# Kernel optimization log

Hardware: AMD Instinct MI355X
Metric: run time of the kernel (lower is better)

Reference implementation:

```python
import jax, jax.numpy as jnp
import numpy as np

DIM = 1024; DEPTH = 4; HEADS = 16; DIM_HEAD = 64
INNER = HEADS * DIM_HEAD            # 1024
N_LAT = 64; N_MP = 4; MAX_SEQ = 512
FF_MULT = 4; HID = DIM * FF_MULT    # 4096
B = 32; SEQ = 512
EPS = 1e-5


def _custom_ln(x, g):
    # LayerNorm with gain only (module's custom LayerNorm), biased variance
    mean = x.mean(-1, keepdims=True)
    var = x.var(-1, keepdims=True)
    return (x - mean) * jax.lax.rsqrt(var + EPS) * g


def _std_ln(x, w, b):
    # torch nn.LayerNorm with weight and bias
    mean = x.mean(-1, keepdims=True)
    var = x.var(-1, keepdims=True)
    return (x - mean) * jax.lax.rsqrt(var + EPS) * w + b


def setup_inputs() -> dict:
    key = jax.random.key(0)
    ks = jax.random.split(key, 12)
    w = lambda k, shape: jax.random.normal(k, shape, jnp.float32) * 0.02
    return {
        "x": jax.random.normal(ks[0], (B, SEQ, DIM), jnp.float32),
        "mask": jnp.ones((B, SEQ), dtype=bool),
        "pos_emb": w(ks[1], (MAX_SEQ, DIM)),
        "latents": jax.random.normal(ks[2], (N_LAT, DIM), jnp.float32),
        "mp_ln_g": jnp.ones((DIM,), jnp.float32),
        "mp_w": w(ks[3], (DIM, DIM * N_MP)),
        "mp_b": jnp.zeros((DIM * N_MP,), jnp.float32),
        "attn_norm_w": jnp.ones((DEPTH, DIM), jnp.float32),
        "attn_norm_b": jnp.zeros((DEPTH, DIM), jnp.float32),
        "attn_lat_w": jnp.ones((DEPTH, DIM), jnp.float32),
        "attn_lat_b": jnp.zeros((DEPTH, DIM), jnp.float32),
        "Wq": w(ks[4], (DEPTH, DIM, INNER)),
        "Wkv": w(ks[5], (DEPTH, DIM, 2 * INNER)),
        "Wout": w(ks[6], (DEPTH, INNER, DIM)),
        "out_ln_w": jnp.ones((DEPTH, DIM), jnp.float32),
        "out_ln_b": jnp.zeros((DEPTH, DIM), jnp.float32),
        "ff_ln1_g": jnp.ones((DEPTH, DIM), jnp.float32),
        "ff_w1": w(ks[7], (DEPTH, DIM, HID)),
        "ff_ln2_g": jnp.ones((DEPTH, HID), jnp.float32),
        "ff_w2": w(ks[8], (DEPTH, HID, DIM)),
    }


def _forward(x, mask, pos_emb, latents, mp_ln_g, mp_w, mp_b,
             attn_norm_w, attn_norm_b, attn_lat_w, attn_lat_b,
             Wq, Wkv, Wout, out_ln_w, out_ln_b,
             ff_ln1_g, ff_w1, ff_ln2_g, ff_w2):
    b, n, d = x.shape
    x_pos = x + pos_emb[:n]                              # [b, n, d]
    lat = jnp.broadcast_to(latents, (b,) + latents.shape)  # [b, 64, d]

    # latents from mean-pooled sequence (mask in torch code is all-ones)
    pooled = x.mean(axis=1)                              # [b, d]
    mp_lat = (_custom_ln(pooled, mp_ln_g) @ mp_w + mp_b).reshape(b, N_MP, d)
    lat = jnp.concatenate([mp_lat, lat], axis=1)         # [b, 68, d]
    n_lat = lat.shape[1]

    scale = DIM_HEAD ** -0.5
    pad_mask = jnp.pad(mask, ((0, 0), (0, n_lat)), constant_values=True)  # [b, n+68]
    neg = -jnp.finfo(jnp.float32).max

    def split_heads(t):
        return t.reshape(b, -1, HEADS, DIM_HEAD).transpose(0, 2, 1, 3)  # b h n d

    for i in range(DEPTH):
        # --- PerceiverAttention ---
        xn = _std_ln(x_pos, attn_norm_w[i], attn_norm_b[i])
        ln_ = _std_ln(lat, attn_lat_w[i], attn_lat_b[i])
        q = split_heads(ln_ @ Wq[i]) * scale
        kv = jnp.concatenate([xn, ln_], axis=1) @ Wkv[i]   # [b, n+68, 2*inner]
        k, v = jnp.split(kv, 2, axis=-1)
        k = split_heads(k); v = split_heads(v)
        sim = jnp.einsum('bhid,bhjd->bhij', q, k)          # [b, h, 68, n+68]
        sim = jnp.where(pad_mask[:, None, None, :], sim, neg)
        attn = jax.nn.softmax(sim.astype(jnp.float32), axis=-1).astype(sim.dtype)
        out = jnp.einsum('bhij,bhjd->bhid', attn, v)
        out = out.transpose(0, 2, 1, 3).reshape(b, n_lat, INNER)
        lat = _std_ln(out @ Wout[i], out_ln_w[i], out_ln_b[i]) + lat
        # --- FeedForward ---
        h = _custom_ln(lat, ff_ln1_g[i]) @ ff_w1[i]
        h = jax.nn.gelu(h, approximate=False)              # torch nn.GELU default
        h = _custom_ln(h, ff_ln2_g[i]) @ ff_w2[i]
        lat = h + lat
    return lat


def reference(x, mask, pos_emb, latents, mp_ln_g, mp_w, mp_b,
              attn_norm_w, attn_norm_b, attn_lat_w, attn_lat_b,
              Wq, Wkv, Wout, out_ln_w, out_ln_b,
              ff_ln1_g, ff_w1, ff_ln2_g, ff_w2):
    return _forward(x, mask, pos_emb, latents, mp_ln_g, mp_w, mp_b,
                    attn_norm_w, attn_norm_b, attn_lat_w, attn_lat_b,
                    Wq, Wkv, Wout, out_ln_w, out_ln_b,
                    ff_ln1_g, ff_w1, ff_ln2_g, ff_w2)
```

## Files before the change

### kernel.cpp

```cpp
#include <hip/hip_runtime.h>


typedef __attribute__((ext_vector_type(4))) float f32x4;
typedef __attribute__((ext_vector_type(8))) __bf16 bf16x8;
typedef __attribute__((ext_vector_type(4))) __bf16 bf16x4;

#define BATCH 32
#define SEQL  512
#define DIM   1024
#define HEADS 16
#define DH    64
#define LTOT  68
#define KEYS  580
#define KPAD  640
#define HID   4096
#define LN_EPS 1e-5f
#define MLAT  2176

__device__ __forceinline__ float bf2f(__bf16 v) { return (float)v; }
__device__ __forceinline__ __bf16 f2bf(float v) { return (__bf16)v; }
__device__ __forceinline__ float gelu_f(float v) {
    return 0.5f * v * (1.0f + erff(v * 0.70710678118654752f));
}

__device__ __forceinline__ void gld_lds16(const __bf16* g, __bf16* l) {
    __builtin_amdgcn_global_load_lds(
        (const __attribute__((address_space(1))) void*)g,
        (__attribute__((address_space(3))) void*)l, 16, 0, 0);
}

#define SBAR()   asm volatile("s_barrier" ::: "memory")
#define VMCNT4() asm volatile("s_waitcnt vmcnt(4)" ::: "memory")

__device__ __forceinline__ void block_reduce2(float& a, float& b, float* red) {
#pragma unroll
    for (int m = 32; m > 0; m >>= 1) {
        a += __shfl_xor(a, m, 64);
        b += __shfl_xor(b, m, 64);
    }
    int wid = threadIdx.x >> 6, lane = threadIdx.x & 63;
    __syncthreads();
    if (lane == 0) { red[wid] = a; red[4 + wid] = b; }
    __syncthreads();
    a = red[0] + red[1] + red[2] + red[3];
    b = red[4] + red[5] + red[6] + red[7];
}

__global__ __launch_bounds__(256) void add_pos(const float* __restrict__ x,
                                               const float* __restrict__ pos,
                                               __bf16* __restrict__ xp) {
    const int total4 = (BATCH * SEQL * DIM) / 4;
    const int pos4m = (SEQL * DIM) / 4 - 1;
    for (int i = blockIdx.x * 256 + threadIdx.x; i < total4; i += gridDim.x * 256) {
        f32x4 xv = ((const f32x4*)x)[i];
        f32x4 pv = ((const f32x4*)pos)[i & pos4m];
        bf16x4 o;
#pragma unroll
        for (int j = 0; j < 4; ++j) o[j] = f2bf(xv[j] + pv[j]);
        ((bf16x4*)xp)[i] = o;
    }
}

__global__ __launch_bounds__(256) void pool_mean(const float* __restrict__ x,
                                                 float* __restrict__ pooled) {
    int b = blockIdx.x >> 2;
    int d = ((blockIdx.x & 3) << 8) + threadIdx.x;
    const float* p = x + (size_t)b * SEQL * DIM + d;
    float s = 0.f;
    for (int ss = 0; ss < SEQL; ++ss) s += p[(size_t)ss * DIM];
    pooled[b * DIM + d] = s * (1.f / SEQL);
}

__global__ __launch_bounds__(256) void lat_fill(const float* __restrict__ latents,
                                                float* __restrict__ lat) {
    int i = blockIdx.x * 256 + threadIdx.x;
    int b = i >> 14;
    int rem = i & 16383;
    int r = rem >> 8, d4 = rem & 255;
    ((f32x4*)lat)[(size_t)(b * LTOT + 4 + r) * 256 + d4] = ((const f32x4*)latents)[rem];
}

template <typename Tin, bool STD, int COLS>
__global__ __launch_bounds__(256) void ln_rows(const Tin* __restrict__ in,
                                               __bf16* __restrict__ out,
                                               const float* __restrict__ w,
                                               const float* __restrict__ bb) {
    __shared__ float red[8];
    constexpr int NPT = COLS / 256;
    size_t base = (size_t)blockIdx.x * COLS;
    int t = threadIdx.x;
    int c0 = t * NPT;
    float xv[NPT];
    float s = 0.f, s2 = 0.f;
#pragma unroll
    for (int k4 = 0; k4 < NPT / 4; ++k4) {
        if constexpr (sizeof(Tin) == 2) {
            bf16x4 v = *(const bf16x4*)(in + base + c0 + k4 * 4);
#pragma unroll
            for (int e = 0; e < 4; ++e) {
                float f = bf2f(v[e]);
                xv[k4 * 4 + e] = f; s += f; s2 += f * f;
            }
        } else {
            f32x4 v = *(const f32x4*)((const float*)in + base + c0 + k4 * 4);
#pragma unroll
            for (int e = 0; e < 4; ++e) {
                float f = v[e];
                xv[k4 * 4 + e] = f; s += f; s2 += f * f;
            }
        }
    }
    block_reduce2(s, s2, red);
    float mean = s * (1.f / COLS);
    float var = s2 * (1.f / COLS) - mean * mean;
    float rstd = rsqrtf(var + LN_EPS);
#pragma unroll
    for (int k4 = 0; k4 < NPT / 4; ++k4) {
        f32x4 wv = *(const f32x4*)(w + c0 + k4 * 4);
        f32x4 bv;
        if (STD) bv = *(const f32x4*)(bb + c0 + k4 * 4);
        bf16x4 o;
#pragma unroll
        for (int e = 0; e < 4; ++e) {
            float y = (xv[k4 * 4 + e] - mean) * rstd * wv[e];
            if (STD) y += bv[e];
            o[e] = f2bf(y);
        }
        *(bf16x4*)(out + base + c0 + k4 * 4) = o;
    }
}

__global__ __launch_bounds__(256) void ln_gelu2(const __bf16* __restrict__ pk,
                                                __bf16* __restrict__ out,
                                                const float* __restrict__ g) {
    __shared__ float red[8];
    constexpr int NPT = HID / 256;
    const size_t S = (size_t)MLAT * HID;
    size_t base = (size_t)blockIdx.x * HID;
    int t = threadIdx.x;
    int c0 = t * NPT;
    float xv[NPT];
    float s = 0.f, s2 = 0.f;
#pragma unroll
    for (int k4 = 0; k4 < NPT / 4; ++k4) {
        bf16x4 va = *(const bf16x4*)(pk + base + c0 + k4 * 4);
        bf16x4 vb = *(const bf16x4*)(pk + S + base + c0 + k4 * 4);
#pragma unroll
        for (int e = 0; e < 4; ++e) {
            float f = gelu_f(bf2f(va[e]) + bf2f(vb[e]));
            xv[k4 * 4 + e] = f; s += f; s2 += f * f;
        }
    }
    block_reduce2(s, s2, red);
    float mean = s * (1.f / HID);
    float var = s2 * (1.f / HID) - mean * mean;
    float rstd = rsqrtf(var + LN_EPS);
#pragma unroll
    for (int k4 = 0; k4 < NPT / 4; ++k4) {
        f32x4 gv = *(const f32x4*)(g + c0 + k4 * 4);
        bf16x4 o;
#pragma unroll
        for (int e = 0; e < 4; ++e)
            o[e] = f2bf((xv[k4 * 4 + e] - mean) * rstd * gv[e]);
        *(bf16x4*)(out + base + c0 + k4 * 4) = o;
    }
}

__global__ __launch_bounds__(256) void wout_ln_res(const __bf16* __restrict__ gin,
                                                   float* __restrict__ lat,
                                                   __bf16* __restrict__ ffin,
                                                   const float* __restrict__ w,
                                                   const float* __restrict__ b,
                                                   const float* __restrict__ g1) {
    __shared__ float red[8];
    const size_t SL = (size_t)MLAT * DIM;
    size_t base = (size_t)blockIdx.x * DIM;
    int t = threadIdx.x;
    float xv[4];
    float s = 0.f, s2 = 0.f;
#pragma unroll
    for (int k = 0; k < 4; ++k) {
        size_t idx = base + t + (k << 8);
        float v = bf2f(gin[idx]) + bf2f(gin[idx + SL]) +
                  bf2f(gin[idx + 2 * SL]) + bf2f(gin[idx + 3 * SL]);
        xv[k] = v; s += v; s2 += v * v;
    }
    block_reduce2(s, s2, red);
    float mean = s * (1.f / DIM);
    float var = s2 * (1.f / DIM) - mean * mean;
    float rstd = rsqrtf(var + LN_EPS);
    float yv[4];
    s = 0.f; s2 = 0.f;
#pragma unroll
    for (int k = 0; k < 4; ++k) {
        int c = t + (k << 8);
        float y = (xv[k] - mean) * rstd * w[c] + b[c] + lat[base + c];
        yv[k] = y; s += y; s2 += y * y;
        lat[base + c] = y;
    }
    block_reduce2(s, s2, red);
    float mean2 = s * (1.f / DIM);
    float var2 = s2 * (1.f / DIM) - mean2 * mean2;
    float rstd2 = rsqrtf(var2 + LN_EPS);
#pragma unroll
    for (int k = 0; k < 4; ++k) {
        int c = t + (k << 8);
        ffin[base + c] = f2bf((yv[k] - mean2) * rstd2 * g1[c]);
    }
}

__global__ __launch_bounds__(256) void qkv_red(const __bf16* __restrict__ pk,
                                               __bf16* __restrict__ qb,
                                               __bf16* __restrict__ kvb) {
    const size_t S = (size_t)MLAT * 3072;
    int row = blockIdx.y;
    int n = (blockIdx.x * 256 + threadIdx.x) * 4;
    size_t idx = (size_t)row * 3072 + n;
    bf16x4 a = *(const bf16x4*)(pk + idx);
    bf16x4 b = *(const bf16x4*)(pk + S + idx);
    bf16x4 o;
    if (n < 1024) {
#pragma unroll
        for (int e = 0; e < 4; ++e) o[e] = f2bf((bf2f(a[e]) + bf2f(b[e])) * 0.125f);
        *(bf16x4*)(qb + (size_t)row * 1024 + n) = o;
    } else {
#pragma unroll
        for (int e = 0; e < 4; ++e) o[e] = f2bf(bf2f(a[e]) + bf2f(b[e]));
        int bb = ((row >> 2) * 61681) >> 20;
        int r = row - bb * 68;
        *(bf16x4*)(kvb + (size_t)bb * KEYS * 2048 + (size_t)(512 + r) * 2048 +
                   (n - 1024)) = o;
    }
}

__global__ __launch_bounds__(256) void splitk_add8(const __bf16* __restrict__ p,
                                                   float* __restrict__ lat) {
    const size_t S = (size_t)MLAT * 1024;
    int i = blockIdx.x * 256 + threadIdx.x;
    size_t e0 = (size_t)i * 4;
    f32x4 acc = ((f32x4*)lat)[i];
#pragma unroll
    for (int s = 0; s < 8; ++s) {
        bf16x4 v = *(const bf16x4*)(p + s * S + e0);
#pragma unroll
        for (int e = 0; e < 4; ++e) acc[e] += bf2f(v[e]);
    }
    ((f32x4*)lat)[i] = acc;
}

__global__ __launch_bounds__(256) void transpose_all(
    const float* __restrict__ Wq, const float* __restrict__ Wkv,
    const float* __restrict__ Wout, const float* __restrict__ f1,
    const float* __restrict__ f2,
    __bf16* __restrict__ wqT, __bf16* __restrict__ wkvT,
    __bf16* __restrict__ woutT, __bf16* __restrict__ f1T,
    __bf16* __restrict__ f2T) {
    __shared__ float tile[32][33];
    int bid = blockIdx.x;
    const float* in; __bf16* out; int N, nxs, ti;
    if (bid < 1024)      { in = Wq;  out = wqT;  N = 1024; nxs = 5; ti = bid; }
    else if (bid < 3072) { in = Wkv; out = wkvT; N = 2048; nxs = 6; ti = bid - 1024; }
    else if (bid < 4096) { in = Wout;out = woutT;N = 1024; nxs = 5; ti = bid - 3072; }
    else if (bid < 8192) { in = f1;  out = f1T;  N = 4096; nxs = 7; ti = bid - 4096; }
    else                 { in = f2;  out = f2T;  N = 1024; nxs = 5; ti = bid - 8192; }
    int K = (bid >= 8192) ? 4096 : 1024;
    int n0 = (ti & ((1 << nxs) - 1)) << 5;
    int k0 = (ti >> nxs) << 5;
    int tx = threadIdx.x & 31, ty = threadIdx.x >> 5;
#pragma unroll
    for (int p = 0; p < 4; ++p) {
        int kk = ty + p * 8;
        tile[kk][tx] = in[(size_t)(k0 + kk) * N + n0 + tx];
    }
    __syncthreads();
#pragma unroll
    for (int p = 0; p < 4; ++p) {
        int nn = ty + p * 8;
        out[(size_t)(n0 + nn) * K + k0 + tx] = f2bf(tile[tx][nn]);
    }
}

__global__ __launch_bounds__(256) void transpose_cast(const float* __restrict__ in,
                                                      __bf16* __restrict__ out,
                                                      int K, int N) {
    __shared__ float tile[32][33];
    int n0 = blockIdx.x * 32, k0 = blockIdx.y * 32;
    int tx = threadIdx.x & 31, ty = threadIdx.x >> 5;
#pragma unroll
    for (int p = 0; p < 4; ++p) {
        int kk = ty + p * 8;
        tile[kk][tx] = in[(size_t)(k0 + kk) * N + n0 + tx];
    }
    __syncthreads();
#pragma unroll
    for (int p = 0; p < 4; ++p) {
        int nn = ty + p * 8;
        out[(size_t)(n0 + nn) * K + k0 + tx] = f2bf(tile[tx][nn]);
    }
}

template <int EPI, bool POW2>
__global__ __launch_bounds__(256) void gemm_bf16(
    const __bf16* __restrict__ A, const __bf16* __restrict__ Bt,
    void* __restrict__ C0, void* __restrict__ C1, const float* __restrict__ bias,
    int M, int N, int K, int lda, int ldb, int brs, long long bstride, int ldc,
    float scale, int az, long long cz, int zhalf) {
    __shared__ __bf16 As[128][64];
    __shared__ __bf16 Bs[128][64];
    const int t = threadIdx.x;
    const int m0 = blockIdx.y * 128, n0 = blockIdx.x * 128;
    const int z = blockIdx.z;
    A += (size_t)z * az;
    Bt += (size_t)z * az;
    void* Cout = (z < zhalf) ? C0 : C1;
    const long long zoff = (long long)(z < zhalf ? z : z - zhalf) * cz;
    const int wid = t >> 6, lane = t & 63;
    const int wr = wid >> 1, wc = wid & 1;
    const int lrow = lane & 15;
    const int lr = lane >> 3, lc = lane & 7;
    const int src_col = (lc ^ lr) << 3;
    f32x4 acc[4][4] = {};

    int garow[4], gbrow[4];
#pragma unroll
    for (int it = 0; it < 4; ++it) {
        int r = wid * 8 + it * 32 + lr;
        int gm = m0 + r; garow[it] = gm < M ? gm : M - 1;
        int gn = n0 + r; gbrow[it] = gn < N ? gn : N - 1;
    }

    for (int kt = 0; kt < K; kt += 64) {
#pragma unroll
        for (int it = 0; it < 4; ++it) {
            int rb = wid * 8 + it * 32;
            gld_lds16(A + (size_t)garow[it] * lda + kt + src_col, &As[rb][0]);
            gld_lds16(Bt + (size_t)gbrow[it] * ldb + kt + src_col, &Bs[rb][0]);
        }
        __syncthreads();
#pragma unroll
        for (int kc = 0; kc < 2; ++kc) {
            const int ck = (kc << 2) + (lane >> 4);
            bf16x8 af[4], bfr[4];
#pragma unroll
            for (int f = 0; f < 4; ++f) {
                int ra = wr * 64 + f * 16 + lrow;
                af[f] = *(const bf16x8*)(&As[ra][(ck ^ (ra & 7)) << 3]);
                int rb = wc * 64 + f * 16 + lrow;
                bfr[f] = *(const bf16x8*)(&Bs[rb][(ck ^ (rb & 7)) << 3]);
            }
#pragma unroll
            for (int fm = 0; fm < 4; ++fm)
#pragma unroll
                for (int fn = 0; fn < 4; ++fn)
                    acc[fm][fn] = __builtin_amdgcn_mfma_f32_16x16x32_bf16(
                        af[fm], bfr[fn], acc[fm][fn], 0, 0, 0);
        }
        __syncthreads();
    }
    const int rbase = (lane >> 4) << 2;
    const int cofs = lane & 15;
    const int msk = POW2 ? (int)((1u << brs) - 1u) : 0;
#pragma unroll
    for (int fm = 0; fm < 4; ++fm) {
#pragma unroll
        for (int j = 0; j < 4; ++j) {
            int m = m0 + wr * 64 + fm * 16 + rbase + j;
            if (m >= M) continue;
            long long roff;
            if (POW2) roff = (long long)(m >> brs) * bstride + (long long)(m & msk) * ldc;
            else      roff = (long long)(m / brs) * bstride + (long long)(m % brs) * ldc;
            roff += zoff;
#pragma unroll
            for (int fn = 0; fn < 4; ++fn) {
                int n = n0 + wc * 64 + fn * 16 + cofs;
                if (n >= N) continue;
                float v = acc[fm][fn][j];
                if (bias) v += bias[n];
                if (EPI == 0) ((float*)Cout)[roff + n] = v;
                else if (EPI == 1) ((__bf16*)Cout)[roff + n] = f2bf(v);
                else if (EPI == 2) ((__bf16*)Cout)[roff + n] = f2bf(v * scale);
                else ((float*)Cout)[roff + n] = gelu_f(v);
            }
        }
    }
}

template <int EPI>
__global__ __launch_bounds__(512, 2) void gemm256(
    const __bf16* __restrict__ A, const __bf16* __restrict__ Bt,
    void* __restrict__ Cout, const float* __restrict__ bias,
    int M, int N, int K, int brs, long long bstride, int ldc, float scale,
    int gxs) {
    __shared__ __bf16 As[2][256][64];
    __shared__ __bf16 Bs[2][256][64];
    const int t = threadIdx.x;
    const int wid = t >> 6, lane = t & 63;
    const int wr = wid >> 2, wc = wid & 3;
    const int lrow = lane & 15, lk = lane >> 4;
    const int lr8 = lane >> 3;
    const int scol = ((lane & 7) ^ lr8) << 3;

    int nwg = gridDim.x;
    int L = blockIdx.x;
    if ((nwg & 7) == 0) L = (L & 7) * (nwg >> 3) + (L >> 3);
    const int bx = L & ((1 << gxs) - 1), by = L >> gxs;
    const int m0 = by * 256, n0 = bx * 256;

    unsigned aoff[4], boff[4];
#pragma unroll
    for (int h = 0; h < 2; ++h)
#pragma unroll
        for (int rnd = 0; rnd < 2; ++rnd) {
            int r = h * 128 + rnd * 64 + wid * 8 + lr8;
            int gm = m0 + r; if (gm > M - 1) gm = M - 1;
            aoff[h * 2 + rnd] = (unsigned)(gm * K + scol);
            int gn = n0 + r; if (gn > N - 1) gn = N - 1;
            boff[h * 2 + rnd] = (unsigned)(gn * K + scol);
        }

    auto stgA = [&](int buf, int tile, int h) {
        int kt = tile << 6;
        gld_lds16(A + aoff[h * 2 + 0] + kt, &As[buf][h * 128 + wid * 8][0]);
        gld_lds16(A + aoff[h * 2 + 1] + kt, &As[buf][h * 128 + 64 + wid * 8][0]);
    };
    auto stgB = [&](int buf, int tile, int h) {
        int kt = tile << 6;
        gld_lds16(Bt + boff[h * 2 + 0] + kt, &Bs[buf][h * 128 + wid * 8][0]);
        gld_lds16(Bt + boff[h * 2 + 1] + kt, &Bs[buf][h * 128 + 64 + wid * 8][0]);
    };

    f32x4 acc[8][4] = {};
    bf16x8 AF0[4][2], AF1[4][2], BF[2][2], BF2[2][2];

    auto rdAF = [&](bf16x8 (&AF)[4][2], int buf, int qm) {
#pragma unroll
        for (int i = 0; i < 4; ++i) {
            int ra = wr * 128 + (qm * 4 + i) * 16 + lrow;
            AF[i][0] = *(const bf16x8*)(&As[buf][ra][((lk) ^ (ra & 7)) << 3]);
            AF[i][1] = *(const bf16x8*)(&As[buf][ra][((4 + lk) ^ (ra & 7)) << 3]);
        }
    };
    auto rdBF = [&](bf16x8 (&BV)[2][2], int buf, int qn) {
#pragma unroll
        for (int i = 0; i < 2; ++i) {
            int rb = wc * 64 + (qn * 2 + i) * 16 + lrow;
            BV[i][0] = *(const bf16x8*)(&Bs[buf][rb][((lk) ^ (rb & 7)) << 3]);
            BV[i][1] = *(const bf16x8*)(&Bs[buf][rb][((4 + lk) ^ (rb & 7)) << 3]);
        }
    };
    auto mfq = [&](bf16x8 (&AF)[4][2], bf16x8 (&BV)[2][2], int mo, int no) {
        __builtin_amdgcn_s_setprio(1);
#pragma unroll
        for (int i = 0; i < 4; ++i)
#pragma unroll
            for (int nf = 0; nf < 2; ++nf)
#pragma unroll
                for (int ks = 0; ks < 2; ++ks)
                    acc[mo + i][no + nf] = __builtin_amdgcn_mfma_f32_16x16x32_bf16(
                        AF[i][ks], BV[nf][ks], acc[mo + i][no + nf], 0, 0, 0);
        __builtin_amdgcn_s_setprio(0);
    };

    const int nt = K >> 6;
    stgA(0, 0, 0); stgA(0, 0, 1);
    stgB(0, 0, 0); stgB(0, 0, 1);
    stgA(1, 1, 0); stgA(1, 1, 1);
    VMCNT4();
    SBAR();

    for (int tt = 0; tt < nt; tt += 2) {
        const int t1 = tt + 1;
        const int t2 = (tt + 2 < nt) ? tt + 2 : nt - 1;
        const int t3 = (tt + 3 < nt) ? tt + 3 : nt - 1;
        rdAF(AF0, 0, 0); rdBF(BF, 0, 0);
        stgB(1, t1, 0);
        SBAR();
        mfq(AF0, BF, 0, 0);
        SBAR();
        rdAF(AF1, 0, 1);
        stgB(1, t1, 1);
        SBAR();
        mfq(AF1, BF, 4, 0);
        SBAR();
        rdBF(BF2, 0, 1);
        stgA(0, t2, 0);
        SBAR();
        mfq(AF1, BF2, 4, 2);
        SBAR();
        stgA(0, t2, 1);
        SBAR();
        mfq(AF0, BF2, 0, 2);
        VMCNT4();
        SBAR();
        rdAF(AF0, 1, 0); rdBF(BF, 1, 0);
        stgB(0, t2, 0);
        SBAR();
        mfq(AF0, BF, 0, 0);
        SBAR();
        rdAF(AF1, 1, 1);
        stgB(0, t2, 1);
        SBAR();
        mfq(AF1, BF, 4, 0);
        SBAR();
        rdBF(BF2, 1, 1);
        stgA(1, t3, 0);
        SBAR();
        mfq(AF1, BF2, 4, 2);
        SBAR();
        stgA(1, t3, 1);
        SBAR();
        mfq(AF0, BF2, 0, 2);
        VMCNT4();
        SBAR();
    }

    const int rbase = (lane >> 4) << 2;
    const int cofs = lane & 15;
    const int msk = (int)((1u << brs) - 1u);
#pragma unroll
    for (int mf = 0; mf < 8; ++mf) {
#pragma unroll
        for (int j = 0; j < 4; ++j) {
            int m = m0 + wr * 128 + mf * 16 + rbase + j;
            if (m >= M) continue;
            long long roff = (long long)(m >> brs) * bstride +
                             (long long)(m & msk) * ldc;
#pragma unroll
            for (int nf = 0; nf < 4; ++nf) {
                int n = n0 + wc * 64 + nf * 16 + cofs;
                if (n >= N) continue;
                float v = acc[mf][nf][j];
                if (bias) v += bias[n];
                if (EPI == 1) ((__bf16*)Cout)[roff + n] = f2bf(v);
                else if (EPI == 3) ((float*)Cout)[roff + n] = gelu_f(v);
                else ((float*)Cout)[roff + n] = v;
            }
        }
    }
}

__global__ __launch_bounds__(256) void qk_gemm(const __bf16* __restrict__ q,
                                               const __bf16* __restrict__ kv,
                                               __bf16* __restrict__ sp) {
    __shared__ __bf16 Qs[80][64];
    __shared__ __bf16 Ks[128][64];
    const int bh = blockIdx.x, b = bh >> 4, h = bh & 15;
    const int n0 = blockIdx.y * 128;
    const int t = threadIdx.x, wid = t >> 6, lane = t & 63;
    const __bf16* qbase = q + (size_t)b * LTOT * DIM + h * DH;
    const __bf16* kbase = kv + (size_t)b * KEYS * 2048 + h * DH;
    const bf16x8 zero8 = {};

    for (int s = t; s < 80 * 8; s += 256) {
        int r = s >> 3, c8 = s & 7;
        bf16x8 v = zero8;
        if (r < LTOT) v = *(const bf16x8*)(qbase + (size_t)r * DIM + (c8 << 3));
        *(bf16x8*)(&Qs[r][(c8 ^ (r & 7)) << 3]) = v;
    }
    for (int s = t; s < 128 * 8; s += 256) {
        int r = s >> 3, c8 = s & 7;
        int gk = n0 + r; if (gk >= KEYS) gk = KEYS - 1;
        bf16x8 v = *(const bf16x8*)(kbase + (size_t)gk * 2048 + (c8 << 3));
        *(bf16x8*)(&Ks[r][(c8 ^ (r & 7)) << 3]) = v;
    }
    __syncthreads();

    const int lrow = lane & 15;
    f32x4 acc[5][2] = {};
#pragma unroll
    for (int kc = 0; kc < 2; ++kc) {
        const int ck = (kc << 2) + (lane >> 4);
        bf16x8 bfr[2];
#pragma unroll
        for (int fn = 0; fn < 2; ++fn) {
            int rb = wid * 32 + fn * 16 + lrow;
            bfr[fn] = *(const bf16x8*)(&Ks[rb][(ck ^ (rb & 7)) << 3]);
        }
#pragma unroll
        for (int fm = 0; fm < 5; ++fm) {
            int ra = fm * 16 + lrow;
            bf16x8 af = *(const bf16x8*)(&Qs[ra][(ck ^ (ra & 7)) << 3]);
#pragma unroll
            for (int fn = 0; fn < 2; ++fn)
                acc[fm][fn] = __builtin_amdgcn_mfma_f32_16x16x32_bf16(
                    af, bfr[fn], acc[fm][fn], 0, 0, 0);
        }
    }
    __bf16* srow = sp + (size_t)bh * LTOT * KPAD;
    const int rbase = (lane >> 4) << 2, cofs = lane & 15;
#pragma unroll
    for (int fm = 0; fm < 5; ++fm)
#pragma unroll
        for (int j = 0; j < 4; ++j) {
            int r = fm * 16 + rbase + j;
            if (r >= LTOT) continue;
#pragma unroll
            for (int fn = 0; fn < 2; ++fn) {
                int col = n0 + wid * 32 + fn * 16 + cofs;
                srow[(size_t)r * KPAD + col] = f2bf(acc[fm][fn][j]);
            }
        }
}

__global__ __launch_bounds__(256) void softmax_p(__bf16* __restrict__ sp) {
    const int row = blockIdx.x * 4 + (threadIdx.x >> 6);
    const int lane = threadIdx.x & 63;
    __bf16* p = sp + (size_t)row * KPAD;
    float v[10];
    float m = -3.0e38f;
#pragma unroll
    for (int i = 0; i < 10; ++i) {
        int c = (i << 6) + lane;
        float f = (c < KEYS) ? bf2f(p[c]) : -3.0e38f;
        v[i] = f; m = fmaxf(m, f);
    }
#pragma unroll
    for (int mk = 32; mk > 0; mk >>= 1) m = fmaxf(m, __shfl_xor(m, mk, 64));
    float l = 0.f;
#pragma unroll
    for (int i = 0; i < 10; ++i) {
        int c = (i << 6) + lane;
        float e = (c < KEYS) ? __expf(v[i] - m) : 0.f;
        v[i] = e; l += e;
    }
#pragma unroll
    for (int mk = 32; mk > 0; mk >>= 1) l += __shfl_xor(l, mk, 64);
    float inv = 1.f / l;
#pragma unroll
    for (int i = 0; i < 10; ++i) {
        int c = (i << 6) + lane;
        p[c] = f2bf(v[i] * inv);
    }
}

__global__ __launch_bounds__(256) void vt_tr(const __bf16* __restrict__ kv,
                                             __bf16* __restrict__ vt) {
    __shared__ __bf16 tile[32][34];
    const int bh = blockIdx.x, b = bh >> 4, h = bh & 15;
    const int k0 = blockIdx.y * 32, d0 = blockIdx.z * 32;
    const int tx = threadIdx.x & 31, ty = threadIdx.x >> 5;
    const __bf16* vbase = kv + (size_t)b * KEYS * 2048 + 1024 + h * DH;
#pragma unroll
    for (int p = 0; p < 4; ++p) {
        int kk = k0 + ty + p * 8;
        int kc = kk < KEYS ? kk : KEYS - 1;
        tile[ty + p * 8][tx] = vbase[(size_t)kc * 2048 + d0 + tx];
    }
    __syncthreads();
    __bf16* obase = vt + (size_t)bh * DH * KPAD;
#pragma unroll
    for (int p = 0; p < 4; ++p) {
        int nn = ty + p * 8;
        __bf16 val = (k0 + tx < KEYS) ? tile[tx][nn] : (__bf16)0.f;
        obase[(size_t)(d0 + nn) * KPAD + k0 + tx] = val;
    }
}

__global__ __launch_bounds__(256) void pv_gemm(const __bf16* __restrict__ sp,
                                               const __bf16* __restrict__ vt,
                                               __bf16* __restrict__ ao) {
    __shared__ __bf16 Ps[80][64];
    __shared__ __bf16 Vs[64][64];
    const int bh = blockIdx.x, b = bh >> 4, h = bh & 15;
    const int t = threadIdx.x, wid = t >> 6, lane = t & 63;
    const int lrow = lane & 15;
    const __bf16* pbase = sp + (size_t)bh * LTOT * KPAD;
    const __bf16* vbase = vt + (size_t)bh * DH * KPAD;
    const bf16x8 zero8 = {};
    f32x4 acc[5] = {};

    for (int kt = 0; kt < KPAD; kt += 64) {
        for (int s = t; s < 80 * 8; s += 256) {
            int r = s >> 3, c8 = s & 7;
            bf16x8 v = zero8;
            if (r < LTOT) v = *(const bf16x8*)(pbase + (size_t)r * KPAD + kt + (c8 << 3));
            *(bf16x8*)(&Ps[r][(c8 ^ (r & 7)) << 3]) = v;
        }
        for (int s = t; s < 64 * 8; s += 256) {
            int r = s >> 3, c8 = s & 7;
            bf16x8 v = *(const bf16x8*)(vbase + (size_t)r * KPAD + kt + (c8 << 3));
            *(bf16x8*)(&Vs[r][(c8 ^ (r & 7)) << 3]) = v;
        }
        __syncthreads();
#pragma unroll
        for (int kc = 0; kc < 2; ++kc) {
            const int ck = (kc << 2) + (lane >> 4);
            int rb = wid * 16 + lrow;
            bf16x8 bfr = *(const bf16x8*)(&Vs[rb][(ck ^ (rb & 7)) << 3]);
#pragma unroll
            for (int fm = 0; fm < 5; ++fm) {
                int ra = fm * 16 + lrow;
                bf16x8 af = *(const bf16x8*)(&Ps[ra][(ck ^ (ra & 7)) << 3]);
                acc[fm] = __builtin_amdgcn_mfma_f32_16x16x32_bf16(
                    af, bfr, acc[fm], 0, 0, 0);
            }
        }
        __syncthreads();
    }
    __bf16* obase = ao + (size_t)b * LTOT * DIM + h * DH;
    const int rbase = (lane >> 4) << 2, cofs = lane & 15;
#pragma unroll
    for (int fm = 0; fm < 5; ++fm)
#pragma unroll
        for (int j = 0; j < 4; ++j) {
            int r = fm * 16 + rbase + j;
            if (r >= LTOT) continue;
            obase[(size_t)r * DIM + wid * 16 + cofs] = f2bf(acc[fm][j]);
        }
}

template <int EPI, bool POW2>
static void g128(const __bf16* A, const __bf16* Bt, void* C0, void* C1,
                 const float* bias, int M, int N, int K, int lda, int ldb,
                 int brs, long long bs, int ldc, float scale, int gz, int az,
                 long long cz, int zhalf, hipStream_t s) {
    dim3 g(N / 128, (M + 127) / 128, gz);
    gemm_bf16<EPI, POW2><<<g, 256, 0, s>>>(A, Bt, C0, C1, bias, M, N, K, lda,
                                           ldb, brs, bs, ldc, scale, az, cz,
                                           zhalf);
}

extern "C" void kernel_launch(void* const* d_in, const int* in_sizes, int n_in,
                              void* d_out, int out_size, void* d_ws, size_t ws_size,
                              hipStream_t stream) {
    (void)in_sizes; (void)n_in; (void)out_size; (void)ws_size;
    const float* x          = (const float*)d_in[0];
    const float* pos_emb    = (const float*)d_in[2];
    const float* latents    = (const float*)d_in[3];
    const float* mp_ln_g    = (const float*)d_in[4];
    const float* mp_w       = (const float*)d_in[5];
    const float* mp_b       = (const float*)d_in[6];
    const float* attn_norm_w= (const float*)d_in[7];
    const float* attn_norm_b= (const float*)d_in[8];
    const float* attn_lat_w = (const float*)d_in[9];
    const float* attn_lat_b = (const float*)d_in[10];
    const float* Wq         = (const float*)d_in[11];
    const float* Wkv        = (const float*)d_in[12];
    const float* Wout       = (const float*)d_in[13];
    const float* out_ln_w   = (const float*)d_in[14];
    const float* out_ln_b   = (const float*)d_in[15];
    const float* ff_ln1_g   = (const float*)d_in[16];
    const float* ff_w1      = (const float*)d_in[17];
    const float* ff_ln2_g   = (const float*)d_in[18];
    const float* ff_w2      = (const float*)d_in[19];

    float* lat = (float*)d_out;

    char* ws = (char*)d_ws;
    size_t off = 0;
    auto take = [&](size_t bytes) -> char* {
        char* p = ws + off;
        off += (bytes + 255) & ~(size_t)255;
        return p;
    };
    __bf16* xpos = (__bf16*)take(2ULL * BATCH * SEQL * DIM);
    __bf16* xn   = (__bf16*)take(2ULL * BATCH * SEQL * DIM);
    __bf16* lnl  = (__bf16*)take(2ULL * BATCH * LTOT * DIM);
    __bf16* ffin = (__bf16*)take(2ULL * BATCH * LTOT * DIM);
    __bf16* qb   = (__bf16*)take(2ULL * BATCH * LTOT * DIM);
    __bf16* ao   = (__bf16*)take(2ULL * BATCH * LTOT * DIM);
    __bf16* kvb  = (__bf16*)take(2ULL * BATCH * KEYS * 2048);
    float*  gout = (float*)take(4ULL * MLAT * HID);
    __bf16* h2   = (__bf16*)take(2ULL * MLAT * HID);
    __bf16* vt   = (__bf16*)take(2ULL * BATCH * HEADS * DH * KPAD);
    __bf16* wT   = (__bf16*)take(2ULL * 12 * 1024 * 1024);
    float*  pooled = (float*)take(4ULL * BATCH * DIM);
    __bf16* mpin = (__bf16*)take(2ULL * BATCH * DIM);

    __bf16* sp  = (__bf16*)gout;
    __bf16* gkb = (__bf16*)gout;

    __bf16* wqT   = wT;
    __bf16* wkvT  = wT + 1 * 1024 * 1024;
    __bf16* woutT = wT + 3 * 1024 * 1024;
    __bf16* f1T   = wT + 4 * 1024 * 1024;
    __bf16* f2T   = wT + 8 * 1024 * 1024;
    __bf16* mpwT  = wT;

    add_pos<<<4096, 256, 0, stream>>>(x, pos_emb, xpos);
    pool_mean<<<128, 256, 0, stream>>>(x, pooled);
    ln_rows<float, false, DIM><<<BATCH, 256, 0, stream>>>(pooled, mpin, mp_ln_g, nullptr);
    transpose_cast<<<dim3(128, 32), 256, 0, stream>>>(mp_w, mpwT, 1024, 4096);
    g128<0, true>(mpin, mpwT, lat, lat, mp_b, BATCH, 4096, 1024, 1024, 1024,
                  5, 0, LTOT * DIM, 1.f, 1, 0, 0, 1, stream);
    lat_fill<<<2048, 256, 0, stream>>>(latents, lat);

    for (int i = 0; i < 4; ++i) {
        transpose_all<<<12288, 256, 0, stream>>>(
            Wq + (size_t)i * 1024 * 1024, Wkv + (size_t)i * 1024 * 2048,
            Wout + (size_t)i * 1024 * 1024, ff_w1 + (size_t)i * 1024 * 4096,
            ff_w2 + (size_t)i * 4096 * 1024,
            wqT, wkvT, woutT, f1T, f2T);

        ln_rows<__bf16, true, DIM><<<BATCH * SEQL, 256, 0, stream>>>(
            xpos, xn, attn_norm_w + i * DIM, attn_norm_b + i * DIM);
        ln_rows<float, true, DIM><<<BATCH * LTOT, 256, 0, stream>>>(
            lat, lnl, attn_lat_w + i * DIM, attn_lat_b + i * DIM);

        g128<1, true>(lnl, wqT, gkb, gkb, nullptr, MLAT, 3072, 512, 1024, 1024,
                      31, 0, 3072, 1.f, 2, 512, (long long)MLAT * 3072, 2, stream);
        qkv_red<<<dim3(3, MLAT), 256, 0, stream>>>(gkb, qb, kvb);

        gemm256<1><<<dim3(512), 512, 0, stream>>>(
            xn, wkvT, kvb, nullptr, BATCH * SEQL, 2048, 1024,
            9, (long long)KEYS * 2048, 2048, 1.f, 3);

        vt_tr<<<dim3(BATCH * HEADS, KPAD / 32, 2), 256, 0, stream>>>(kvb, vt);
        qk_gemm<<<dim3(BATCH * HEADS, KPAD / 128), 256, 0, stream>>>(qb, kvb, sp);
        softmax_p<<<(BATCH * HEADS * LTOT) / 4, 256, 0, stream>>>(sp);
        pv_gemm<<<BATCH * HEADS, 256, 0, stream>>>(sp, vt, ao);

        g128<1, true>(ao, woutT, vt, vt, nullptr, MLAT, 1024, 256, 1024, 1024,
                      31, 0, 1024, 1.f, 4, 256, (long long)MLAT * 1024, 4, stream);
        wout_ln_res<<<BATCH * LTOT, 256, 0, stream>>>(
            vt, lat, ffin, out_ln_w + i * DIM, out_ln_b + i * DIM, ff_ln1_g + i * DIM);

        g128<1, true>(ffin, f1T, gkb, gkb, nullptr, MLAT, HID, 512, 1024, 1024,
                      31, 0, HID, 1.f, 2, 512, (long long)MLAT * HID, 2, stream);
        ln_gelu2<<<BATCH * LTOT, 256, 0, stream>>>(gkb, h2, ff_ln2_g + i * HID);

        g128<1, true>(h2, f2T, gkb, gkb, nullptr, MLAT, 1024, 512, HID, HID,
                      31, 0, 1024, 1.f, 8, 512, (long long)MLAT * 1024, 8, stream);
        splitk_add8<<<MLAT, 256, 0, stream>>>(gkb, lat);
    }
}
```

Baseline: 1.659 ms.

## Fuse QK GEMM, softmax and PV GEMM into one attention kernel

Replaces the separate qk_gemm, softmax_p and pv_gemm kernels with a single fused_attn kernel per (batch, head). The score matrix is kept in LDS (80x640 bf16), along with the row max and row sum, instead of round-tripping through global memory. K and V tiles are double-buffered via direct global-to-LDS loads. Normalisation is deferred to the output write. This removes two launches and the global traffic for the score matrix. In exchange, the large LDS footprint limits occupancy, and the QK phase now runs in one block per head rather than five.

```diff
diff --git a/kernel.cpp b/kernel.cpp
--- a/kernel.cpp
+++ b/kernel.cpp
@@ -539,100 +539,6 @@
     }
 }
 
-__global__ __launch_bounds__(256) void qk_gemm(const __bf16* __restrict__ q,
-                                               const __bf16* __restrict__ kv,
-                                               __bf16* __restrict__ sp) {
-    __shared__ __bf16 Qs[80][64];
-    __shared__ __bf16 Ks[128][64];
-    const int bh = blockIdx.x, b = bh >> 4, h = bh & 15;
-    const int n0 = blockIdx.y * 128;
-    const int t = threadIdx.x, wid = t >> 6, lane = t & 63;
-    const __bf16* qbase = q + (size_t)b * LTOT * DIM + h * DH;
-    const __bf16* kbase = kv + (size_t)b * KEYS * 2048 + h * DH;
-    const bf16x8 zero8 = {};
-
-    for (int s = t; s < 80 * 8; s += 256) {
-        int r = s >> 3, c8 = s & 7;
-        bf16x8 v = zero8;
-        if (r < LTOT) v = *(const bf16x8*)(qbase + (size_t)r * DIM + (c8 << 3));
-        *(bf16x8*)(&Qs[r][(c8 ^ (r & 7)) << 3]) = v;
-    }
-    for (int s = t; s < 128 * 8; s += 256) {
-        int r = s >> 3, c8 = s & 7;
-        int gk = n0 + r; if (gk >= KEYS) gk = KEYS - 1;
-        bf16x8 v = *(const bf16x8*)(kbase + (size_t)gk * 2048 + (c8 << 3));
-        *(bf16x8*)(&Ks[r][(c8 ^ (r & 7)) << 3]) = v;
-    }
-    __syncthreads();
-
-    const int lrow = lane & 15;
-    f32x4 acc[5][2] = {};
-#pragma unroll
-    for (int kc = 0; kc < 2; ++kc) {
-        const int ck = (kc << 2) + (lane >> 4);
-        bf16x8 bfr[2];
-#pragma unroll
-        for (int fn = 0; fn < 2; ++fn) {
-            int rb = wid * 32 + fn * 16 + lrow;
-            bfr[fn] = *(const bf16x8*)(&Ks[rb][(ck ^ (rb & 7)) << 3]);
-        }
-#pragma unroll
-        for (int fm = 0; fm < 5; ++fm) {
-            int ra = fm * 16 + lrow;
-            bf16x8 af = *(const bf16x8*)(&Qs[ra][(ck ^ (ra & 7)) << 3]);
-#pragma unroll
-            for (int fn = 0; fn < 2; ++fn)
-                acc[fm][fn] = __builtin_amdgcn_mfma_f32_16x16x32_bf16(
-                    af, bfr[fn], acc[fm][fn], 0, 0, 0);
-        }
-    }
-    __bf16* srow = sp + (size_t)bh * LTOT * KPAD;
-    const int rbase = (lane >> 4) << 2, cofs = lane & 15;
-#pragma unroll
-    for (int fm = 0; fm < 5; ++fm)
-#pragma unroll
-        for (int j = 0; j < 4; ++j) {
-            int r = fm * 16 + rbase + j;
-            if (r >= LTOT) continue;
-#pragma unroll
-            for (int fn = 0; fn < 2; ++fn) {
-                int col = n0 + wid * 32 + fn * 16 + cofs;
-                srow[(size_t)r * KPAD + col] = f2bf(acc[fm][fn][j]);
-            }
-        }
-}
-
-__global__ __launch_bounds__(256) void softmax_p(__bf16* __restrict__ sp) {
-    const int row = blockIdx.x * 4 + (threadIdx.x >> 6);
-    const int lane = threadIdx.x & 63;
-    __bf16* p = sp + (size_t)row * KPAD;
-    float v[10];
-    float m = -3.0e38f;
-#pragma unroll
-    for (int i = 0; i < 10; ++i) {
-        int c = (i << 6) + lane;
-        float f = (c < KEYS) ? bf2f(p[c]) : -3.0e38f;
-        v[i] = f; m = fmaxf(m, f);
-    }
-#pragma unroll
-    for (int mk = 32; mk > 0; mk >>= 1) m = fmaxf(m, __shfl_xor(m, mk, 64));
-    float l = 0.f;
-#pragma unroll
-    for (int i = 0; i < 10; ++i) {
-        int c = (i << 6) + lane;
-        float e = (c < KEYS) ? __expf(v[i] - m) : 0.f;
-        v[i] = e; l += e;
-    }
-#pragma unroll
-    for (int mk = 32; mk > 0; mk >>= 1) l += __shfl_xor(l, mk, 64);
-    float inv = 1.f / l;
-#pragma unroll
-    for (int i = 0; i < 10; ++i) {
-        int c = (i << 6) + lane;
-        p[c] = f2bf(v[i] * inv);
-    }
-}
-
 __global__ __launch_bounds__(256) void vt_tr(const __bf16* __restrict__ kv,
                                              __bf16* __restrict__ vt) {
     __shared__ __bf16 tile[32][34];
@@ -656,56 +562,163 @@
     }
 }
 
-__global__ __launch_bounds__(256) void pv_gemm(const __bf16* __restrict__ sp,
-                                               const __bf16* __restrict__ vt,
-                                               __bf16* __restrict__ ao) {
-    __shared__ __bf16 Ps[80][64];
-    __shared__ __bf16 Vs[64][64];
+__global__ __launch_bounds__(256) void fused_attn(const __bf16* __restrict__ q,
+                                                  const __bf16* __restrict__ kv,
+                                                  const __bf16* __restrict__ vt,
+                                                  __bf16* __restrict__ ao) {
+    __shared__ __bf16 Qs[80][64];
+    __shared__ __bf16 Ks[2][64][64];
+    __shared__ __bf16 Ps[80][640];
+    __shared__ float rowpm[4][80];
+    __shared__ float rowm[80];
+    __shared__ float rowl[80];
+
     const int bh = blockIdx.x, b = bh >> 4, h = bh & 15;
-    const int t = threadIdx.x, wid = t >> 6, lane = t & 63;
+    const int t = threadIdx.x, w = t >> 6, lane = t & 63;
     const int lrow = lane & 15;
-    const __bf16* pbase = sp + (size_t)bh * LTOT * KPAD;
+    const int rbase = (lane >> 4) << 2, cofs = lane & 15;
+    const int lr = lane >> 3, lc = lane & 7;
+    const int src_col = (lc ^ lr) << 3;
+
+    const __bf16* qbase = q + (size_t)b * LTOT * DIM + h * DH;
+    const bf16x8 zero8 = {};
+    for (int s = t; s < 80 * 8; s += 256) {
+        int r = s >> 3, c8 = s & 7;
+        bf16x8 v = zero8;
+        if (r < LTOT) v = *(const bf16x8*)(qbase + (size_t)r * DIM + (c8 << 3));
+        *(bf16x8*)(&Qs[r][(c8 ^ (r & 7)) << 3]) = v;
+    }
+
+    const __bf16* kbase = kv + (size_t)b * KEYS * 2048 + h * DH;
     const __bf16* vbase = vt + (size_t)bh * DH * KPAD;
-    const bf16x8 zero8 = {};
-    f32x4 acc[5] = {};
-
-    for (int kt = 0; kt < KPAD; kt += 64) {
-        for (int s = t; s < 80 * 8; s += 256) {
-            int r = s >> 3, c8 = s & 7;
-            bf16x8 v = zero8;
-            if (r < LTOT) v = *(const bf16x8*)(pbase + (size_t)r * KPAD + kt + (c8 << 3));
-            *(bf16x8*)(&Ps[r][(c8 ^ (r & 7)) << 3]) = v;
-        }
-        for (int s = t; s < 64 * 8; s += 256) {
-            int r = s >> 3, c8 = s & 7;
-            bf16x8 v = *(const bf16x8*)(vbase + (size_t)r * KPAD + kt + (c8 << 3));
-            *(bf16x8*)(&Vs[r][(c8 ^ (r & 7)) << 3]) = v;
-        }
-        __syncthreads();
+
+    auto stageK = [&](int buf, int kt) {
+#pragma unroll
+        for (int rnd = 0; rnd < 2; ++rnd) {
+            int r8 = w * 16 + rnd * 8;
+            int gk = kt * 64 + r8 + lr; if (gk > KEYS - 1) gk = KEYS - 1;
+            gld_lds16(kbase + (size_t)gk * 2048 + src_col, &Ks[buf][r8][0]);
+        }
+    };
+    auto stageV = [&](int buf, int kt) {
+#pragma unroll
+        for (int rnd = 0; rnd < 2; ++rnd) {
+            int r8 = w * 16 + rnd * 8;
+            gld_lds16(vbase + (size_t)(r8 + lr) * KPAD + kt * 64 + src_col,
+                      &Ks[buf][r8][0]);
+        }
+    };
+
+    float pmax[5][4];
+#pragma unroll
+    for (int fm = 0; fm < 5; ++fm)
+#pragma unroll
+        for (int j = 0; j < 4; ++j) pmax[fm][j] = -3.0e38f;
+
+    stageK(0, 0);
+    __syncthreads();
+    for (int kt = 0; kt < 10; ++kt) {
+        if (kt < 9) stageK((kt + 1) & 1, kt + 1);
+        f32x4 acc[5] = {};
 #pragma unroll
         for (int kc = 0; kc < 2; ++kc) {
-            const int ck = (kc << 2) + (lane >> 4);
-            int rb = wid * 16 + lrow;
-            bf16x8 bfr = *(const bf16x8*)(&Vs[rb][(ck ^ (rb & 7)) << 3]);
+            int ck = (kc << 2) + (lane >> 4);
+            int rb = w * 16 + lrow;
+            bf16x8 bfr = *(const bf16x8*)(&Ks[kt & 1][rb][(ck ^ (rb & 7)) << 3]);
 #pragma unroll
             for (int fm = 0; fm < 5; ++fm) {
                 int ra = fm * 16 + lrow;
-                bf16x8 af = *(const bf16x8*)(&Ps[ra][(ck ^ (ra & 7)) << 3]);
+                bf16x8 af = *(const bf16x8*)(&Qs[ra][(ck ^ (ra & 7)) << 3]);
                 acc[fm] = __builtin_amdgcn_mfma_f32_16x16x32_bf16(
                     af, bfr, acc[fm], 0, 0, 0);
             }
         }
+        int key = kt * 64 + w * 16 + cofs;
+        int c8 = key >> 3, e = key & 7;
+#pragma unroll
+        for (int fm = 0; fm < 5; ++fm) {
+#pragma unroll
+            for (int j = 0; j < 4; ++j) {
+                int qrow = fm * 16 + rbase + j;
+                float v = (key < KEYS) ? acc[fm][j] : -1.0e30f;
+                pmax[fm][j] = fmaxf(pmax[fm][j], v);
+                int swz = ((c8 & 7) ^ (qrow & 7)) | (c8 & ~7);
+                Ps[qrow][swz * 8 + e] = f2bf(v);
+            }
+        }
         __syncthreads();
     }
+#pragma unroll
+    for (int fm = 0; fm < 5; ++fm)
+#pragma unroll
+        for (int j = 0; j < 4; ++j) {
+            float m = pmax[fm][j];
+            m = fmaxf(m, __shfl_xor(m, 1, 64));
+            m = fmaxf(m, __shfl_xor(m, 2, 64));
+            m = fmaxf(m, __shfl_xor(m, 4, 64));
+            m = fmaxf(m, __shfl_xor(m, 8, 64));
+            if (cofs == 0) rowpm[w][fm * 16 + rbase + j] = m;
+        }
+    __syncthreads();
+    if (t < 80)
+        rowm[t] = fmaxf(fmaxf(rowpm[0][t], rowpm[1][t]),
+                        fmaxf(rowpm[2][t], rowpm[3][t]));
+    __syncthreads();
+
+    for (int rr = t >> 2; rr < LTOT; rr += 64) {
+        int c4 = t & 3;
+        float m = rowm[rr];
+        float lsum = 0.f;
+#pragma unroll
+        for (int cc = 0; cc < 20; ++cc) {
+            int c8 = c4 * 20 + cc;
+            int swz = ((c8 & 7) ^ (rr & 7)) | (c8 & ~7);
+            bf16x8 v = *(bf16x8*)(&Ps[rr][swz * 8]);
+            bf16x8 o;
+#pragma unroll
+            for (int e = 0; e < 8; ++e) {
+                float p = __expf(bf2f(v[e]) - m);
+                lsum += p;
+                o[e] = f2bf(p);
+            }
+            *(bf16x8*)(&Ps[rr][swz * 8]) = o;
+        }
+        lsum += __shfl_xor(lsum, 1, 64);
+        lsum += __shfl_xor(lsum, 2, 64);
+        if (c4 == 0) rowl[rr] = lsum;
+    }
+
+    stageV(0, 0);
+    __syncthreads();
+    f32x4 oacc[5] = {};
+    for (int kt = 0; kt < 10; ++kt) {
+        if (kt < 9) stageV((kt + 1) & 1, kt + 1);
+#pragma unroll
+        for (int kc = 0; kc < 2; ++kc) {
+            int ck = (kc << 2) + (lane >> 4);
+            int rb = w * 16 + lrow;
+            bf16x8 bfr = *(const bf16x8*)(&Ks[kt & 1][rb][(ck ^ (rb & 7)) << 3]);
+            int gc8 = kt * 8 + ck;
+#pragma unroll
+            for (int fm = 0; fm < 5; ++fm) {
+                int ra = fm * 16 + lrow;
+                int swz = ((gc8 & 7) ^ (ra & 7)) | (gc8 & ~7);
+                bf16x8 af = *(const bf16x8*)(&Ps[ra][swz * 8]);
+                oacc[fm] = __builtin_amdgcn_mfma_f32_16x16x32_bf16(
+                    af, bfr, oacc[fm], 0, 0, 0);
+            }
+        }
+        __syncthreads();
+    }
     __bf16* obase = ao + (size_t)b * LTOT * DIM + h * DH;
-    const int rbase = (lane >> 4) << 2, cofs = lane & 15;
 #pragma unroll
     for (int fm = 0; fm < 5; ++fm)
 #pragma unroll
         for (int j = 0; j < 4; ++j) {
-            int r = fm * 16 + rbase + j;
-            if (r >= LTOT) continue;
-            obase[(size_t)r * DIM + wid * 16 + cofs] = f2bf(acc[fm][j]);
+            int qrow = fm * 16 + rbase + j;
+            if (qrow >= LTOT) continue;
+            float inv = 1.f / rowl[qrow];
+            obase[(size_t)qrow * DIM + w * 16 + cofs] = f2bf(oacc[fm][j] * inv);
         }
 }
 
@@ -767,7 +780,6 @@
     float*  pooled = (float*)take(4ULL * BATCH * DIM);
     __bf16* mpin = (__bf16*)take(2ULL * BATCH * DIM);
 
-    __bf16* sp  = (__bf16*)gout;
     __bf16* gkb = (__bf16*)gout;
 
     __bf16* wqT   = wT;
@@ -806,9 +818,7 @@
             9, (long long)KEYS * 2048, 2048, 1.f, 3);
 
         vt_tr<<<dim3(BATCH * HEADS, KPAD / 32, 2), 256, 0, stream>>>(kvb, vt);
-        qk_gemm<<<dim3(BATCH * HEADS, KPAD / 128), 256, 0, stream>>>(qb, kvb, sp);
-        softmax_p<<<(BATCH * HEADS * LTOT) / 4, 256, 0, stream>>>(sp);
-        pv_gemm<<<BATCH * HEADS, 256, 0, stream>>>(sp, vt, ao);
+        fused_attn<<<BATCH * HEADS, 256, 0, stream>>>(qb, kvb, vt, ao);
 
         g128<1, true>(ao, woutT, vt, vt, nullptr, MLAT, 1024, 256, 1024, 1024,
                       31, 0, 1024, 1.f, 4, 256, (long long)MLAT * 1024, 4, stream);
```

New measurement: 1.678 ms (median of 2 runs). About the same (+1.2%).
